# Performance work log

Measured on AMD Instinct MI355X. Metric: run time of the kernel, lower is better.

The kernel has to match this reference:

```python
import jax, jax.numpy as jnp
import numpy as np

B, T, C = 2, 2048, 2048
H, KV, D = 16, 4, 128   # n_head, n_kv_head, head_dim
EPS = 1.1920929e-07     # torch.finfo(float32).eps, F.rms_norm default


def setup_inputs() -> dict:
    key = jax.random.key(0)
    ks = jax.random.split(key, 7)
    x = jax.random.normal(ks[0], (B, T, C), dtype=jnp.float32)
    # rope angles: cos/sin of positions, broadcastable to [B,T,H,D//2]
    inv_freq = 1.0 / (10000.0 ** (jnp.arange(0, D // 2, dtype=jnp.float32) / (D // 2)))
    ang = jnp.arange(T, dtype=jnp.float32)[:, None] * inv_freq[None, :]
    cos = jnp.cos(ang)[None, :, None, :]  # [1,T,1,D/2]
    sin = jnp.sin(ang)[None, :, None, :]
    s = 0.02
    Wq = jax.random.normal(ks[1], (C, H * D), dtype=jnp.float32) * s
    Wk = jax.random.normal(ks[2], (C, KV * D), dtype=jnp.float32) * s
    Wv = jax.random.normal(ks[3], (C, KV * D), dtype=jnp.float32) * s
    Wo = jax.random.normal(ks[4], (C, C), dtype=jnp.float32) * s
    return {"x": x, "cos": cos, "sin": sin, "Wq": Wq, "Wk": Wk, "Wv": Wv, "Wo": Wo}


def _rope(t, cos, sin):
    d = t.shape[-1] // 2
    t1, t2 = t[..., :d], t[..., d:]
    return jnp.concatenate([t1 * cos + t2 * sin, -t1 * sin + t2 * cos], axis=-1)


def _rmsnorm(t):
    return t * jax.lax.rsqrt(jnp.mean(t * t, axis=-1, keepdims=True) + EPS)


def reference(x, cos, sin, Wq, Wk, Wv, Wo):
    q = (x @ Wq).reshape(B, T, H, D)
    k = (x @ Wk).reshape(B, T, KV, D)
    v = (x @ Wv).reshape(B, T, KV, D)
    q = _rmsnorm(_rope(q, cos, sin))
    k = _rmsnorm(_rope(k, cos, sin))
    # [B, KV, G, T, D] query grouped per kv head (GQA)
    G = H // KV
    qh = q.transpose(0, 2, 1, 3).reshape(B, KV, G, T, D)
    kh = k.transpose(0, 2, 1, 3)  # [B, KV, T, D]
    vh = v.transpose(0, 2, 1, 3)
    scale = 1.0 / np.sqrt(D).astype(np.float32)
    scores = jnp.einsum('bhgqd,bhkd->bhgqk', qh, kh) * scale
    causal = jnp.tril(jnp.ones((T, T), dtype=bool))
    scores = jnp.where(causal, scores, jnp.finfo(scores.dtype).min)
    attn = jax.nn.softmax(scores, axis=-1)
    y = jnp.einsum('bhgqk,bhkd->bhgqd', attn, vh)  # [B,KV,G,T,D]
    y = y.reshape(B, H, T, D).transpose(0, 2, 1, 3).reshape(B, T, C)
    return y @ Wo
```

## Files before the change

### kernel.cpp

```cpp
#include <hip/hip_runtime.h>

using bf16x8 = __attribute__((ext_vector_type(8))) short;
using f32x4  = __attribute__((ext_vector_type(4))) float;

#define B_  2
#define T_  2048
#define C_  2048
#define H_  16
#define KV_ 4
#define D_  128

__device__ __forceinline__ unsigned short f2b(float f) {
  union { float f; unsigned int u; } v; v.f = f;
  unsigned int r = v.u + 0x7fffu + ((v.u >> 16) & 1u);
  return (unsigned short)(r >> 16);
}
__device__ __forceinline__ float b2f(unsigned short u) {
  union { unsigned int u; float f; } v; v.u = ((unsigned int)u) << 16;
  return v.f;
}
__device__ __forceinline__ unsigned int cvt_pk_bf16(float lo, float hi) {
  unsigned int r;
  asm("v_cvt_pk_bf16_f32 %0, %1, %2" : "=v"(r) : "v"(lo), "v"(hi));
  return r;
}
__device__ __forceinline__ void gld_lds16(const void* g, void* l) {
  __builtin_amdgcn_global_load_lds(
      (__attribute__((address_space(1))) void*)g,
      (__attribute__((address_space(3))) void*)l, 16, 0, 0);
}

__global__ void cast_bf16_k(const float* __restrict__ in, unsigned short* __restrict__ out) {
  int i = blockIdx.x * 256 + threadIdx.x;
  float4 f = ((const float4*)in)[i];
  ushort4 u; u.x = f2b(f.x); u.y = f2b(f.y); u.z = f2b(f.z); u.w = f2b(f.w);
  ((ushort4*)out)[i] = u;
}

__global__ void wtrans4(const float* __restrict__ Wq, const float* __restrict__ Wk,
                        const float* __restrict__ Wv, const float* __restrict__ Wo,
                        unsigned short* __restrict__ Wqt, unsigned short* __restrict__ Wkt,
                        unsigned short* __restrict__ Wvt, unsigned short* __restrict__ Wot) {
  __shared__ float s[32][33];
  int id = blockIdx.x;
  const float* W; unsigned short* Wt; int N;
  if (id < 4096)      { W = Wq; Wt = Wqt; N = 2048; }
  else if (id < 5120) { W = Wk; Wt = Wkt; N = 512;  id -= 4096; }
  else if (id < 6144) { W = Wv; Wt = Wvt; N = 512;  id -= 5120; }
  else                { W = Wo; Wt = Wot; N = 2048; id -= 6144; }
  int ntiles = N >> 5;
  int n0 = (id % ntiles) * 32, k0 = (id / ntiles) * 32;
  int tx = threadIdx.x, ty = threadIdx.y;
  #pragma unroll
  for (int yy = 0; yy < 32; yy += 8)
    s[ty + yy][tx] = W[(size_t)(k0 + ty + yy) * N + n0 + tx];
  __syncthreads();
  #pragma unroll
  for (int yy = 0; yy < 32; yy += 8)
    Wt[(size_t)(n0 + ty + yy) * 2048 + k0 + tx] = f2b(s[tx][ty + yy]);
}

template <bool OUT_BF16>
__device__ __forceinline__ void gemm_tile(
    const unsigned short* __restrict__ A, const unsigned short* __restrict__ Bt,
    void* __restrict__ Cv, int K, int ldc, int m0, int n0b, int n0c,
    unsigned short* sA, unsigned short* sB)
{
  const int tid  = threadIdx.x;
  const int lane = tid & 63, w = tid >> 6;
  const int quad = lane >> 4, l16 = lane & 15;
  const int wm = (w >> 1) * 64, wn = (w & 1) * 64;

  f32x4 acc[4][4] = {};

  const unsigned short* Abase = A  + (size_t)m0  * K;
  const unsigned short* Bbase = Bt + (size_t)n0b * K;

  for (int k0 = 0; k0 < K; k0 += 32) {
    #pragma unroll
    for (int r = 0; r < 2; ++r) {
      int c = tid + r * 256;
      int row = c >> 2, col = (c & 3) * 8;
      gld_lds16(Abase + (size_t)row * K + k0 + col, sA + c * 8);
      gld_lds16(Bbase + (size_t)row * K + k0 + col, sB + c * 8);
    }
    __syncthreads();
    bf16x8 af[4], bfr[4];
    #pragma unroll
    for (int i = 0; i < 4; ++i)
      af[i]  = *(const bf16x8*)(sA + (wm + i * 16 + l16) * 32 + quad * 8);
    #pragma unroll
    for (int j = 0; j < 4; ++j)
      bfr[j] = *(const bf16x8*)(sB + (wn + j * 16 + l16) * 32 + quad * 8);
    #pragma unroll
    for (int i = 0; i < 4; ++i)
      #pragma unroll
      for (int j = 0; j < 4; ++j)
        acc[i][j] = __builtin_amdgcn_mfma_f32_16x16x32_bf16(af[i], bfr[j], acc[i][j], 0, 0, 0);
    __syncthreads();
  }
  #pragma unroll
  for (int i = 0; i < 4; ++i) {
    #pragma unroll
    for (int r = 0; r < 4; ++r) {
      int row = m0 + wm + i * 16 + quad * 4 + r;
      #pragma unroll
      for (int j = 0; j < 4; ++j) {
        int col = n0c + wn + j * 16 + l16;
        float v = acc[i][j][r];
        if (OUT_BF16) ((unsigned short*)Cv)[(size_t)row * ldc + col] = f2b(v);
        else          ((float*)Cv)[(size_t)row * ldc + col] = v;
      }
    }
  }
}

__global__ void out_gemm(const unsigned short* __restrict__ yb,
                         const unsigned short* __restrict__ Wot,
                         float* __restrict__ out) {
  __shared__ unsigned short sA[128 * 32], sB[128 * 32];
  gemm_tile<false>(yb, Wot, out, C_, C_, blockIdx.y * 128, blockIdx.x * 128, blockIdx.x * 128,
                   sA, sB);
}

__global__ __launch_bounds__(512, 2) void qkv_gemm2p(
    const unsigned short* __restrict__ xb,
    const unsigned short* __restrict__ Wt,
    unsigned short* __restrict__ qkv) {
  __shared__ unsigned short lds[57344];

  const int id  = (int)blockIdx.x;
  const int xcd = id & 7, j = id >> 3;
  const int mt  = xcd * 2 + (j >> 4);
  const int nt  = j & 15;
  const int m0 = mt * 256, n0 = nt * 192;

  const int tid = (int)threadIdx.x;
  const int w = tid >> 6, lane = tid & 63;
  const int quad = lane >> 4, l16 = lane & 15;
  const int wr = w >> 1, wc = w & 1;
  const int swz = (l16 & 12) << 1;

  const unsigned short* Ab = xb + (size_t)m0 * 2048;
  const unsigned short* Bb = Wt + (size_t)n0 * 2048;

  int ar[4], axc[4];
  #pragma unroll
  for (int kq = 0; kq < 4; ++kq) {
    int ca = tid + kq * 512;
    ar[kq]  = (ca & 1023) >> 2;
    axc[kq] = ((ca & 3) * 8) ^ ((((ca & 1023) >> 4) & 3) << 3);
  }
  const int khb1 = (tid < 256) ? 0 : 1;
  int bidx[3] = { tid, tid + 512 - khb1 * 768, tid + 256 };
  int bkh[3]  = { 0, khb1, 1 };
  int br[3], bxc[3];
  #pragma unroll
  for (int kq = 0; kq < 3; ++kq) {
    br[kq]  = bidx[kq] >> 2;
    bxc[kq] = ((bidx[kq] & 3) * 8) ^ (((bidx[kq] >> 4) & 3) << 3);
  }

#define STAGE(buf, kb) do { \
    unsigned short* da_ = lds + (buf) * 16384; \
    _Pragma("unroll") \
    for (int kq = 0; kq < 4; ++kq) { \
      int ca_ = tid + kq * 512; \
      gld_lds16(Ab + (size_t)ar[kq] * 2048 + (kb) + (ca_ >> 10) * 32 + axc[kq], da_ + ca_ * 8); \
    } \
    unsigned short* db_ = lds + 32768 + (buf) * 12288; \
    _Pragma("unroll") \
    for (int kq = 0; kq < 3; ++kq) \
      gld_lds16(Bb + (size_t)br[kq] * 2048 + (kb) + bkh[kq] * 32 + bxc[kq], \
                db_ + bkh[kq] * 6144 + bidx[kq] * 8); \
  } while (0)

  f32x4 acc[4][6] = {};

  STAGE(0, 0);
  __syncthreads();

  const unsigned short* aB = lds + (wr * 64 + l16) * 32 + (quad * 8 ^ swz);
  const unsigned short* bB = lds + 32768 + (wc * 96 + l16) * 32 + (quad * 8 ^ swz);

  for (int t = 0; t < 32; ++t) {
    const int cur = t & 1;
    if (t < 31) STAGE(cur ^ 1, (t + 1) * 64);
    #pragma unroll
    for (int kh = 0; kh < 2; ++kh) {
      bf16x8 a[4], b[6];
      #pragma unroll
      for (int m = 0; m < 4; ++m)
        a[m] = *(const bf16x8*)(aB + cur * 16384 + kh * 8192 + m * 512);
      #pragma unroll
      for (int n = 0; n < 6; ++n)
        b[n] = *(const bf16x8*)(bB + cur * 12288 + kh * 6144 + n * 512);
      #pragma unroll
      for (int m = 0; m < 4; ++m)
        #pragma unroll
        for (int n = 0; n < 6; ++n)
          acc[m][n] = __builtin_amdgcn_mfma_f32_16x16x32_bf16(a[m], b[n], acc[m][n], 0, 0, 0);
    }
    __syncthreads();
  }
#undef STAGE

  #pragma unroll
  for (int m = 0; m < 4; ++m)
    #pragma unroll
    for (int r = 0; r < 4; ++r) {
      int row = m0 + wr * 64 + m * 16 + quad * 4 + r;
      #pragma unroll
      for (int n = 0; n < 6; ++n) {
        int col = n0 + wc * 96 + n * 16 + l16;
        qkv[(size_t)row * 3072 + col] = f2b(acc[m][n][r]);
      }
    }
}

template <int NH>
__global__ void ropenorm(const unsigned short* __restrict__ in,
                         const float* __restrict__ cs, const float* __restrict__ sn,
                         unsigned short* __restrict__ out, float oscale, int ld, int off) {
  int row  = blockIdx.x * 4 + (threadIdx.x >> 6);
  int lane = threadIdx.x & 63;
  int head = row % NH;
  int t = (row / NH) & (T_ - 1);
  int b = row / (NH * T_);
  const unsigned short* p = in + (size_t)(b * T_ + t) * ld + off + head * D_;
  unsigned int u  = *(const unsigned int*)(p + 2 * lane);
  unsigned int up = (unsigned int)__shfl_xor((int)u, 32, 64);
  int dh = (lane & 31) * 2;
  float2 c2 = ((const float2*)(cs + t * 64))[lane & 31];
  float2 s2 = ((const float2*)(sn + t * 64))[lane & 31];
  float a0 = b2f((unsigned short)(u & 0xffff)),  a1 = b2f((unsigned short)(u >> 16));
  float p0 = b2f((unsigned short)(up & 0xffff)), p1 = b2f((unsigned short)(up >> 16));
  float sgn = (lane < 32) ? 1.0f : -1.0f;
  float oa = a0 * c2.x + sgn * p0 * s2.x;
  float ob = a1 * c2.y + sgn * p1 * s2.y;
  float ss = oa * oa + ob * ob;
  #pragma unroll
  for (int off2 = 32; off2 > 0; off2 >>= 1) ss += __shfl_xor(ss, off2, 64);
  float r = rsqrtf(ss * (1.0f / 128.0f) + 1.1920929e-07f) * oscale;
  unsigned int outu = cvt_pk_bf16(oa * r, ob * r);
  size_t base = ((size_t)((b * NH + head) * 128 + (t >> 4))) * 2048 + (size_t)(t & 15) * 8;
  int f = ((lane < 32) ? 0 : 8) + (dh >> 3);
  *(unsigned int*)(out + base + (size_t)f * 128 + (dh & 7)) = outu;
}

__global__ void vfrag_k(const unsigned short* __restrict__ qkv, unsigned short* __restrict__ vf) {
  int it = blockIdx.x;
  int b = blockIdx.y >> 2, kv = blockIdx.y & 3;
  int d = threadIdx.x, ty = threadIdx.y;
  int t0 = it * 64;
  size_t obase = ((size_t)((b * KV_ + kv) * 32 + it)) * 8192
               + (size_t)(d >> 4) * 1024 + (size_t)(d & 15) * 8;
  #pragma unroll
  for (int tcg = 0; tcg < 4; ++tcg) {
    int tc = ty * 4 + tcg;
    unsigned short val[8];
    #pragma unroll
    for (int e = 0; e < 8; ++e)
      val[e] = qkv[((size_t)(b * T_) + t0 + tc * 8 + e) * 3072 + 2560 + kv * D_ + d];
    ushort4 u0 = {val[0], val[1], val[2], val[3]};
    ushort4 u1 = {val[4], val[5], val[6], val[7]};
    *(ushort4*)(vf + obase + (size_t)tc * 128)     = u0;
    *(ushort4*)(vf + obase + (size_t)tc * 128 + 4) = u1;
  }
}

__global__ __launch_bounds__(256, 2) void attn_kernel(
    const unsigned short* __restrict__ qf, const unsigned short* __restrict__ kf,
    const unsigned short* __restrict__ vf, unsigned short* __restrict__ yb) {
  __shared__ __align__(16) char smem[34048];

  const int xp = (int)blockIdx.x;
  const int b = xp >> 2, kv = xp & 3;
  const int yp = (int)blockIdx.y;
  const int j = yp >> 2, hp = yp & 3;
  const int tid = threadIdx.x;
  const int w = tid >> 6, lane = tid & 63;
  const int quad = lane >> 4, l16 = lane & 15;
  const int qsel = w & 1, half = w >> 1;
  const int qt = qsel ? (63 - j) : j;
  const int h = kv * 4 + hp;
  const int q0 = qt * 32;
  const int ntile = (qt >> 1) + 1;
  unsigned short* myP = (unsigned short*)smem + w * (32 * 72);

  const unsigned short* Qf = qf + ((size_t)(b * H_ + h) * 128 + qt * 2) * 2048;
  const unsigned short* Kf = kf + (size_t)(b * KV_ + kv) * 128 * 2048;
  const unsigned short* Vf = vf + (size_t)(b * KV_ + kv) * 32 * 8192;

  bf16x8 bq[2][4];
  #pragma unroll
  for (int i = 0; i < 2; ++i)
    #pragma unroll
    for (int kk = 0; kk < 4; ++kk)
      bq[i][kk] = *(const bf16x8*)(Qf + (size_t)i * 2048 + (kk * 4 + quad) * 128 + l16 * 8);

  float l_i[2] = {0.f, 0.f};
  f32x4 o[2][8] = {};

  for (int it = half; it < ntile; it += 2) {
    const int t0 = it * 64;
    const unsigned short* Kt = Kf + (size_t)(it * 4) * 2048;
    const unsigned short* Vt = Vf + (size_t)it * 8192;

    f32x4 sc[4][2] = {};
    #pragma unroll
    for (int kk = 0; kk < 4; ++kk) {
      bf16x8 ak[4];
      #pragma unroll
      for (int jt = 0; jt < 4; ++jt)
        ak[jt] = *(const bf16x8*)(Kt + (size_t)jt * 2048 + (kk * 4 + quad) * 128 + l16 * 8);
      #pragma unroll
      for (int jt = 0; jt < 4; ++jt)
        #pragma unroll
        for (int i = 0; i < 2; ++i)
          sc[jt][i] = __builtin_amdgcn_mfma_f32_16x16x32_bf16(ak[jt], bq[i][kk], sc[jt][i], 0, 0, 0);
    }

    bf16x8 bv[2][8];
    #pragma unroll
    for (int kk2 = 0; kk2 < 2; ++kk2)
      #pragma unroll
      for (int jj = 0; jj < 8; ++jj)
        bv[kk2][jj] = *(const bf16x8*)(Vt + (size_t)jj * 1024 + (kk2 * 4 + quad) * 128 + l16 * 8);

    if (it == ntile - 1) {
      #pragma unroll
      for (int jt = 0; jt < 4; ++jt) {
        int kg = t0 + jt * 16 + quad * 4;
        #pragma unroll
        for (int i = 0; i < 2; ++i) {
          int qg = q0 + i * 16 + l16;
          #pragma unroll
          for (int r = 0; r < 4; ++r)
            if (kg + r > qg) sc[jt][i][r] = -3.0e38f;
        }
      }
    }

    #pragma unroll
    for (int i = 0; i < 2; ++i) {
      float part = 0.f;
      #pragma unroll
      for (int jt = 0; jt < 4; ++jt)
        #pragma unroll
        for (int r = 0; r < 4; ++r) {
          float p = __expf(sc[jt][i][r] - 12.0f);
          sc[jt][i][r] = p; part += p;
        }
      l_i[i] += part;
    }

    #pragma unroll
    for (int i = 0; i < 2; ++i)
      #pragma unroll
      for (int jt = 0; jt < 4; ++jt) {
        uint2 uu;
        uu.x = cvt_pk_bf16(sc[jt][i][0], sc[jt][i][1]);
        uu.y = cvt_pk_bf16(sc[jt][i][2], sc[jt][i][3]);
        *(uint2*)(myP + (i * 16 + l16) * 72 + jt * 16 + quad * 4) = uu;
      }

    #pragma unroll
    for (int kk2 = 0; kk2 < 2; ++kk2) {
      bf16x8 ap[2];
      #pragma unroll
      for (int i = 0; i < 2; ++i)
        ap[i] = *(const bf16x8*)(myP + (i * 16 + l16) * 72 + kk2 * 32 + quad * 8);
      #pragma unroll
      for (int i = 0; i < 2; ++i)
        #pragma unroll
        for (int jj = 0; jj < 8; ++jj)
          o[i][jj] = __builtin_amdgcn_mfma_f32_16x16x32_bf16(ap[i], bv[kk2][jj], o[i][jj], 0, 0, 0);
    }
  }

  float lsum[2];
  #pragma unroll
  for (int i = 0; i < 2; ++i) {
    float l = l_i[i];
    l += __shfl_xor(l, 16, 64);
    l += __shfl_xor(l, 32, 64);
    lsum[i] = l;
  }

  __syncthreads();
  float* oc = (float*)smem + qsel * (32 * 132);
  float* lc = (float*)smem + 2 * (32 * 132) + qsel * 32;
  if (half == 1) {
    #pragma unroll
    for (int i = 0; i < 2; ++i) {
      if (quad == 0) lc[i * 16 + l16] = lsum[i];
      #pragma unroll
      for (int jj = 0; jj < 8; ++jj)
        #pragma unroll
        for (int r = 0; r < 4; ++r)
          oc[(i * 16 + quad * 4 + r) * 132 + jj * 16 + l16] = o[i][jj][r];
    }
  }
  __syncthreads();
  if (half == 0) {
    #pragma unroll
    for (int i = 0; i < 2; ++i) {
      float l = lsum[i] + lc[i * 16 + l16];
      float linv = 1.0f / l;
      float lr[4];
      #pragma unroll
      for (int r = 0; r < 4; ++r) lr[r] = __shfl(linv, quad * 4 + r, 64);
      #pragma unroll
      for (int r = 0; r < 4; ++r) {
        int tg = q0 + i * 16 + quad * 4 + r;
        unsigned short* yr = yb + (((size_t)(b * T_ + tg)) * H_ + h) * D_;
        #pragma unroll
        for (int jj = 0; jj < 8; ++jj) {
          float vsum = o[i][jj][r] + oc[(i * 16 + quad * 4 + r) * 132 + jj * 16 + l16];
          yr[jj * 16 + l16] = f2b(vsum * lr[r]);
        }
      }
    }
  }
}

extern "C" void kernel_launch(void* const* d_in, const int* in_sizes, int n_in,
                              void* d_out, int out_size, void* d_ws, size_t ws_size,
                              hipStream_t stream) {
  (void)in_sizes; (void)n_in; (void)out_size; (void)ws_size;
  const float* x  = (const float*)d_in[0];
  const float* cs = (const float*)d_in[1];
  const float* sn = (const float*)d_in[2];
  const float* Wq = (const float*)d_in[3];
  const float* Wk = (const float*)d_in[4];
  const float* Wv = (const float*)d_in[5];
  const float* Wo = (const float*)d_in[6];
  float* out = (float*)d_out;
  char* ws = (char*)d_ws;

  unsigned short* xb     = (unsigned short*)(ws + 0);
  unsigned short* Wqkvt  = (unsigned short*)(ws + 16777216);
  unsigned short* Wot    = (unsigned short*)(ws + 29360128);
  unsigned short* qkvcat = (unsigned short*)(ws + 37748736);
  unsigned short* qfr    = (unsigned short*)(ws + 62914560);
  unsigned short* kfr    = (unsigned short*)(ws + 79691776);
  unsigned short* vfr    = (unsigned short*)(ws + 83886080);
  unsigned short* yb     = xb;

  cast_bf16_k<<<dim3(8192), dim3(256), 0, stream>>>(x, xb);
  wtrans4<<<dim3(10240), dim3(32, 8), 0, stream>>>(
      Wq, Wk, Wv, Wo,
      Wqkvt, Wqkvt + (size_t)2048 * 2048, Wqkvt + (size_t)2560 * 2048, Wot);
  qkv_gemm2p<<<dim3(256), dim3(512), 0, stream>>>(xb, Wqkvt, qkvcat);
  ropenorm<16><<<dim3(16384), dim3(256), 0, stream>>>(qkvcat, cs, sn, qfr,
                                                      0.08838834764831845f, 3072, 0);
  ropenorm<4><<<dim3(4096),  dim3(256), 0, stream>>>(qkvcat, cs, sn, kfr, 1.0f, 3072, 2048);
  vfrag_k<<<dim3(32, 8), dim3(128, 2), 0, stream>>>(qkvcat, vfr);
  attn_kernel<<<dim3(8, 128), dim3(256), 0, stream>>>(qfr, kfr, vfr, yb);
  out_gemm<<<dim3(16, 32), dim3(256), 0, stream>>>(yb, Wot, out);
}
```

Baseline: 306.8 us.

## Share K/V tiles across GQA heads via LDS with async double-buffered staging

Restructures the attention kernel so each 512-thread block handles all four query heads of one KV group, processing a light and a heavy causal q-tile in sequence. K and V tiles are now loaded once per block into swizzled LDS with direct global-to-LDS loads. K is double-buffered so the next tile's load overlaps the current compute. This targets the redundant global K/V reads that each head previously did on its own. In exchange it needs about 132KB of LDS, which limits occupancy, and it adds block-wide barriers each iteration.

```diff
diff --git a/kernel.cpp b/kernel.cpp
--- a/kernel.cpp
+++ b/kernel.cpp
@@ -269,160 +269,197 @@
   }
 }
 
-__global__ __launch_bounds__(256, 2) void attn_kernel(
+__global__ __launch_bounds__(512, 2) void attn_kernel(
     const unsigned short* __restrict__ qf, const unsigned short* __restrict__ kf,
     const unsigned short* __restrict__ vf, unsigned short* __restrict__ yb) {
-  __shared__ __align__(16) char smem[34048];
-
-  const int xp = (int)blockIdx.x;
-  const int b = xp >> 2, kv = xp & 3;
-  const int yp = (int)blockIdx.y;
-  const int j = yp >> 2, hp = yp & 3;
-  const int tid = threadIdx.x;
+  __shared__ __align__(16) char smem[135168];
+  unsigned short* kls = (unsigned short*)smem;
+  unsigned short* vls = (unsigned short*)(smem + 65536);
+  unsigned short* Pls = (unsigned short*)(smem + 98304);
+
+  const int xp = (int)blockIdx.x, b = xp >> 2, kv = xp & 3;
+  const int jy = (int)blockIdx.y;
+  const int tid = (int)threadIdx.x;
   const int w = tid >> 6, lane = tid & 63;
   const int quad = lane >> 4, l16 = lane & 15;
-  const int qsel = w & 1, half = w >> 1;
-  const int qt = qsel ? (63 - j) : j;
-  const int h = kv * 4 + hp;
-  const int q0 = qt * 32;
-  const int ntile = (qt >> 1) + 1;
-  unsigned short* myP = (unsigned short*)smem + w * (32 * 72);
-
-  const unsigned short* Qf = qf + ((size_t)(b * H_ + h) * 128 + qt * 2) * 2048;
+  const int hh = w & 3, half = w >> 2;
+  const int h = kv * 4 + hh;
+  unsigned short* myP = Pls + w * (32 * 72);
+
   const unsigned short* Kf = kf + (size_t)(b * KV_ + kv) * 128 * 2048;
   const unsigned short* Vf = vf + (size_t)(b * KV_ + kv) * 32 * 8192;
 
-  bf16x8 bq[2][4];
-  #pragma unroll
-  for (int i = 0; i < 2; ++i)
-    #pragma unroll
-    for (int kk = 0; kk < 4; ++kk)
-      bq[i][kk] = *(const bf16x8*)(Qf + (size_t)i * 2048 + (kk * 4 + quad) * 128 + l16 * 8);
-
-  float l_i[2] = {0.f, 0.f};
-  f32x4 o[2][8] = {};
-
-  for (int it = half; it < ntile; it += 2) {
-    const int t0 = it * 64;
-    const unsigned short* Kt = Kf + (size_t)(it * 4) * 2048;
-    const unsigned short* Vt = Vf + (size_t)it * 8192;
-
-    f32x4 sc[4][2] = {};
-    #pragma unroll
-    for (int kk = 0; kk < 4; ++kk) {
-      bf16x8 ak[4];
-      #pragma unroll
-      for (int jt = 0; jt < 4; ++jt)
-        ak[jt] = *(const bf16x8*)(Kt + (size_t)jt * 2048 + (kk * 4 + quad) * 128 + l16 * 8);
-      #pragma unroll
-      for (int jt = 0; jt < 4; ++jt)
+  const int swl = quad << 4;
+  const int cs0 = (tid * 8) ^ swl;
+  const int cs1 = ((tid + 512) * 8) ^ swl;
+  const int cd0 = tid * 8, cd1 = tid * 8 + 4096;
+
+#define STAGE_K(buf, it0) do { \
+    const unsigned short* s_ = Kf + (size_t)(it0) * 8192; \
+    unsigned short* d_ = kls + (buf) * 16384; \
+    gld_lds16(s_ + cs0, d_ + cd0);               gld_lds16(s_ + cs1, d_ + cd1); \
+    gld_lds16(s_ + 8192 + cs0, d_ + 8192 + cd0); gld_lds16(s_ + 8192 + cs1, d_ + 8192 + cd1); \
+  } while (0)
+#define STAGE_V(it0) do { \
+    const unsigned short* s_ = Vf + (size_t)(it0) * 8192; \
+    gld_lds16(s_ + cs0, vls + cd0);               gld_lds16(s_ + cs1, vls + cd1); \
+    gld_lds16(s_ + 8192 + cs0, vls + 8192 + cd0); gld_lds16(s_ + 8192 + cs1, vls + 8192 + cd1); \
+  } while (0)
+
+  for (int ph = 0; ph < 2; ++ph) {
+    const int qt = ph ? (63 - jy) : jy;
+    const int q0 = qt * 32;
+    const int ntile = (qt >> 1) + 1;
+    const int R = (ntile + 1) >> 1;
+
+    const unsigned short* Qf = qf + ((size_t)(b * H_ + h) * 128 + qt * 2) * 2048;
+    bf16x8 bq[2][4];
+    #pragma unroll
+    for (int i = 0; i < 2; ++i)
+      #pragma unroll
+      for (int kk = 0; kk < 4; ++kk)
+        bq[i][kk] = *(const bf16x8*)(Qf + (size_t)i * 2048 + (kk * 4 + quad) * 128 + l16 * 8);
+
+    float l_i[2] = {0.f, 0.f};
+    f32x4 o[2][8] = {};
+
+    STAGE_K(0, 0);
+
+    for (int r = 0; r < R; ++r) {
+      const int cur = r & 1;
+      const bool more = (r + 1 < R);
+      STAGE_V(2 * r);
+      if (more) STAGE_K(cur ^ 1, 2 * r + 2);
+      if (more) asm volatile("s_waitcnt vmcnt(8)" ::: "memory");
+      else      asm volatile("s_waitcnt vmcnt(4)" ::: "memory");
+      __builtin_amdgcn_s_barrier();
+
+      const int it = 2 * r + half;
+      const bool active = it < ntile;
+      f32x4 sc[4][2] = {};
+      if (active) {
+        const unsigned short* kb = kls + cur * 16384 + half * 8192;
+        #pragma unroll
+        for (int kk = 0; kk < 4; ++kk) {
+          bf16x8 ak[4];
+          #pragma unroll
+          for (int jt = 0; jt < 4; ++jt)
+            ak[jt] = *(const bf16x8*)(kb + ((jt * 2048 + (kk * 4 + quad) * 128 + l16 * 8) ^ swl));
+          #pragma unroll
+          for (int jt = 0; jt < 4; ++jt)
+            #pragma unroll
+            for (int i = 0; i < 2; ++i)
+              sc[jt][i] = __builtin_amdgcn_mfma_f32_16x16x32_bf16(ak[jt], bq[i][kk], sc[jt][i], 0, 0, 0);
+        }
+        if (it == ntile - 1) {
+          #pragma unroll
+          for (int jt = 0; jt < 4; ++jt) {
+            int kg = it * 64 + jt * 16 + quad * 4;
+            #pragma unroll
+            for (int i = 0; i < 2; ++i) {
+              int qg = q0 + i * 16 + l16;
+              #pragma unroll
+              for (int rr = 0; rr < 4; ++rr)
+                if (kg + rr > qg) sc[jt][i][rr] = -3.0e38f;
+            }
+          }
+        }
+        #pragma unroll
+        for (int i = 0; i < 2; ++i) {
+          float part = 0.f;
+          #pragma unroll
+          for (int jt = 0; jt < 4; ++jt)
+            #pragma unroll
+            for (int rr = 0; rr < 4; ++rr) {
+              float p = __expf(sc[jt][i][rr] - 12.0f);
+              sc[jt][i][rr] = p; part += p;
+            }
+          l_i[i] += part;
+        }
         #pragma unroll
         for (int i = 0; i < 2; ++i)
-          sc[jt][i] = __builtin_amdgcn_mfma_f32_16x16x32_bf16(ak[jt], bq[i][kk], sc[jt][i], 0, 0, 0);
-    }
-
-    bf16x8 bv[2][8];
-    #pragma unroll
-    for (int kk2 = 0; kk2 < 2; ++kk2)
-      #pragma unroll
-      for (int jj = 0; jj < 8; ++jj)
-        bv[kk2][jj] = *(const bf16x8*)(Vt + (size_t)jj * 1024 + (kk2 * 4 + quad) * 128 + l16 * 8);
-
-    if (it == ntile - 1) {
-      #pragma unroll
-      for (int jt = 0; jt < 4; ++jt) {
-        int kg = t0 + jt * 16 + quad * 4;
-        #pragma unroll
-        for (int i = 0; i < 2; ++i) {
-          int qg = q0 + i * 16 + l16;
-          #pragma unroll
-          for (int r = 0; r < 4; ++r)
-            if (kg + r > qg) sc[jt][i][r] = -3.0e38f;
+          #pragma unroll
+          for (int jt = 0; jt < 4; ++jt) {
+            uint2 uu;
+            uu.x = cvt_pk_bf16(sc[jt][i][0], sc[jt][i][1]);
+            uu.y = cvt_pk_bf16(sc[jt][i][2], sc[jt][i][3]);
+            *(uint2*)(myP + (i * 16 + l16) * 72 + jt * 16 + quad * 4) = uu;
+          }
+      }
+
+      if (more) asm volatile("s_waitcnt vmcnt(4)" ::: "memory");
+      else      asm volatile("s_waitcnt vmcnt(0)" ::: "memory");
+      __builtin_amdgcn_s_barrier();
+
+      if (active) {
+        const unsigned short* vb = vls + half * 8192;
+        #pragma unroll
+        for (int kk2 = 0; kk2 < 2; ++kk2) {
+          bf16x8 ap[2], bv2[8];
+          #pragma unroll
+          for (int i = 0; i < 2; ++i)
+            ap[i] = *(const bf16x8*)(myP + (i * 16 + l16) * 72 + kk2 * 32 + quad * 8);
+          #pragma unroll
+          for (int jj = 0; jj < 8; ++jj)
+            bv2[jj] = *(const bf16x8*)(vb + ((jj * 1024 + (kk2 * 4 + quad) * 128 + l16 * 8) ^ swl));
+          #pragma unroll
+          for (int i = 0; i < 2; ++i)
+            #pragma unroll
+            for (int jj = 0; jj < 8; ++jj)
+              o[i][jj] = __builtin_amdgcn_mfma_f32_16x16x32_bf16(ap[i], bv2[jj], o[i][jj], 0, 0, 0);
         }
       }
-    }
-
+      __builtin_amdgcn_s_barrier();
+    }
+
+    float lsum[2];
     #pragma unroll
     for (int i = 0; i < 2; ++i) {
-      float part = 0.f;
-      #pragma unroll
-      for (int jt = 0; jt < 4; ++jt)
-        #pragma unroll
-        for (int r = 0; r < 4; ++r) {
-          float p = __expf(sc[jt][i][r] - 12.0f);
-          sc[jt][i][r] = p; part += p;
+      float l = l_i[i];
+      l += __shfl_xor(l, 16, 64);
+      l += __shfl_xor(l, 32, 64);
+      lsum[i] = l;
+    }
+
+    __syncthreads();
+    float* oc = (float*)smem + hh * 4256;
+    float* lc = oc + 32 * 132;
+    if (half == 1) {
+      #pragma unroll
+      for (int i = 0; i < 2; ++i) {
+        if (quad == 0) lc[i * 16 + l16] = lsum[i];
+        #pragma unroll
+        for (int jj = 0; jj < 8; ++jj)
+          #pragma unroll
+          for (int rr = 0; rr < 4; ++rr)
+            oc[(i * 16 + quad * 4 + rr) * 132 + jj * 16 + l16] = o[i][jj][rr];
+      }
+    }
+    __syncthreads();
+    if (half == 0) {
+      #pragma unroll
+      for (int i = 0; i < 2; ++i) {
+        float l = lsum[i] + lc[i * 16 + l16];
+        float linv = 1.0f / l;
+        float lr[4];
+        #pragma unroll
+        for (int rr = 0; rr < 4; ++rr) lr[rr] = __shfl(linv, quad * 4 + rr, 64);
+        #pragma unroll
+        for (int rr = 0; rr < 4; ++rr) {
+          int tg = q0 + i * 16 + quad * 4 + rr;
+          unsigned short* yr = yb + (((size_t)(b * T_ + tg)) * H_ + h) * D_;
+          #pragma unroll
+          for (int jj = 0; jj < 8; ++jj) {
+            float vsum = o[i][jj][rr] + oc[(i * 16 + quad * 4 + rr) * 132 + jj * 16 + l16];
+            yr[jj * 16 + l16] = f2b(vsum * lr[rr]);
+          }
         }
-      l_i[i] += part;
-    }
-
-    #pragma unroll
-    for (int i = 0; i < 2; ++i)
-      #pragma unroll
-      for (int jt = 0; jt < 4; ++jt) {
-        uint2 uu;
-        uu.x = cvt_pk_bf16(sc[jt][i][0], sc[jt][i][1]);
-        uu.y = cvt_pk_bf16(sc[jt][i][2], sc[jt][i][3]);
-        *(uint2*)(myP + (i * 16 + l16) * 72 + jt * 16 + quad * 4) = uu;
-      }
-
-    #pragma unroll
-    for (int kk2 = 0; kk2 < 2; ++kk2) {
-      bf16x8 ap[2];
-      #pragma unroll
-      for (int i = 0; i < 2; ++i)
-        ap[i] = *(const bf16x8*)(myP + (i * 16 + l16) * 72 + kk2 * 32 + quad * 8);
-      #pragma unroll
-      for (int i = 0; i < 2; ++i)
-        #pragma unroll
-        for (int jj = 0; jj < 8; ++jj)
-          o[i][jj] = __builtin_amdgcn_mfma_f32_16x16x32_bf16(ap[i], bv[kk2][jj], o[i][jj], 0, 0, 0);
-    }
-  }
-
-  float lsum[2];
-  #pragma unroll
-  for (int i = 0; i < 2; ++i) {
-    float l = l_i[i];
-    l += __shfl_xor(l, 16, 64);
-    l += __shfl_xor(l, 32, 64);
-    lsum[i] = l;
-  }
-
-  __syncthreads();
-  float* oc = (float*)smem + qsel * (32 * 132);
-  float* lc = (float*)smem + 2 * (32 * 132) + qsel * 32;
-  if (half == 1) {
-    #pragma unroll
-    for (int i = 0; i < 2; ++i) {
-      if (quad == 0) lc[i * 16 + l16] = lsum[i];
-      #pragma unroll
-      for (int jj = 0; jj < 8; ++jj)
-        #pragma unroll
-        for (int r = 0; r < 4; ++r)
-          oc[(i * 16 + quad * 4 + r) * 132 + jj * 16 + l16] = o[i][jj][r];
-    }
-  }
-  __syncthreads();
-  if (half == 0) {
-    #pragma unroll
-    for (int i = 0; i < 2; ++i) {
-      float l = lsum[i] + lc[i * 16 + l16];
-      float linv = 1.0f / l;
-      float lr[4];
-      #pragma unroll
-      for (int r = 0; r < 4; ++r) lr[r] = __shfl(linv, quad * 4 + r, 64);
-      #pragma unroll
-      for (int r = 0; r < 4; ++r) {
-        int tg = q0 + i * 16 + quad * 4 + r;
-        unsigned short* yr = yb + (((size_t)(b * T_ + tg)) * H_ + h) * D_;
-        #pragma unroll
-        for (int jj = 0; jj < 8; ++jj) {
-          float vsum = o[i][jj][r] + oc[(i * 16 + quad * 4 + r) * 132 + jj * 16 + l16];
-          yr[jj * 16 + l16] = f2b(vsum * lr[r]);
-        }
-      }
-    }
-  }
+      }
+    }
+    __syncthreads();
+  }
+#undef STAGE_K
+#undef STAGE_V
 }
 
 extern "C" void kernel_launch(void* const* d_in, const int* in_sizes, int n_in,
@@ -457,6 +494,6 @@
                                                       0.08838834764831845f, 3072, 0);
   ropenorm<4><<<dim3(4096),  dim3(256), 0, stream>>>(qkvcat, cs, sn, kfr, 1.0f, 3072, 2048);
   vfrag_k<<<dim3(32, 8), dim3(128, 2), 0, stream>>>(qkvcat, vfr);
-  attn_kernel<<<dim3(8, 128), dim3(256), 0, stream>>>(qfr, kfr, vfr, yb);
+  attn_kernel<<<dim3(8, 32), dim3(512), 0, stream>>>(qfr, kfr, vfr, yb);
   out_gemm<<<dim3(16, 32), dim3(256), 0, stream>>>(yb, Wot, out);
 }
```

New measurement: 294.2 us. 1.04x faster.
